# Performance work log

Hardware: AMD Instinct MI355X
Metric: run time of the kernel (lower is better)

Reference implementation:

```python
import jax, jax.numpy as jnp
import numpy as np

N_NODES = 100000
N_EDGES = 1600000
D_IN = 64
HID = 64
N_GRAPHS = 64
NEG_SLOPE = 0.2


def _glorot(k, shape):
    s = (6.0 / (shape[-2] + shape[-1])) ** 0.5
    return jax.random.uniform(k, shape, jnp.float32, -s, s)


def setup_inputs() -> dict:
    key = jax.random.key(0)
    ks = jax.random.split(key, 12)
    x = jax.random.normal(ks[0], (N_NODES, D_IN), jnp.float32)
    edge_index = jax.random.randint(ks[1], (2, N_EDGES), 0, N_NODES, dtype=jnp.int32)
    edge_attr = jax.random.normal(ks[2], (N_EDGES,), jnp.float32)
    batch = jnp.sort(jax.random.randint(ks[3], (N_NODES,), 0, N_GRAPHS, dtype=jnp.int32))
    inp = {"x": x, "edge_index": edge_index, "edge_attr": edge_attr, "batch": batch}
    dims = [(D_IN, HID), (HID, HID), (HID, HID)]
    for i, (din, dout) in enumerate(dims):
        inp[f"W{i}"] = _glorot(ks[4 + i], (din, dout))
        # att param is [1, heads=1, 2*out + nb_edge_feats=1] -> flatten to [2*out+1]
        inp[f"att{i}"] = _glorot(ks[7 + i], (1, 2 * dout + 1)).reshape(-1)
        inp[f"b{i}"] = jnp.zeros((dout,), jnp.float32)
    inp["Wf"] = _glorot(ks[10], (HID, 1))
    inp["bf"] = jnp.zeros((1,), jnp.float32)
    return inp


def _gat_layer(h, src, dst, e, valid, W, att, b, n):
    # MyGATConv (heads=1, concat=True): linear, per-edge attention logits,
    # leaky_relu, segment softmax over target nodes, weighted scatter-add.
    C = W.shape[1]
    h = h @ W                                  # [N, C]
    hi = h[dst]                                # gather target features per edge
    hj = h[src]                                # gather source features per edge
    logits = hi @ att[:C] + hj @ att[C:2 * C] + e * att[2 * C]  # [E]
    logits = jnp.where(logits >= 0, logits, NEG_SLOPE * logits)  # leaky_relu
    logits = jnp.where(valid, logits, -jnp.inf)  # drop original self-loops
    m = jax.ops.segment_max(logits, dst, num_segments=n)
    a = jnp.exp(logits - m[dst])
    a = jnp.where(valid, a, 0.0)
    denom = jax.ops.segment_sum(a, dst, num_segments=n)
    a = a / denom[dst]                         # segment softmax (self-loop guarantees denom>0)
    out = jax.ops.segment_sum(hj * a[:, None], dst, num_segments=n)
    return out + b


def reference(x, edge_index, edge_attr, batch, W0, att0, b0, W1, att1, b1, W2, att2, b2, Wf, bf):
    n = x.shape[0]
    src0, dst0 = edge_index[0], edge_index[1]
    loop = jnp.arange(n, dtype=src0.dtype)
    # remove_self_loops (via mask) + add_self_loops with edge_attr fill 0.0
    src = jnp.concatenate([src0, loop])
    dst = jnp.concatenate([dst0, loop])
    e = jnp.concatenate([edge_attr, jnp.zeros((n,), edge_attr.dtype)])
    valid = jnp.concatenate([src0 != dst0, jnp.ones((n,), bool)])
    h = x
    for (W, att, b) in ((W0, att0, b0), (W1, att1, b1), (W2, att2, b2)):
        h = jax.nn.relu(_gat_layer(h, src, dst, e, valid, W, att, b, n))
    pooled = jax.ops.segment_sum(h, batch, num_segments=N_GRAPHS)  # global_add_pool
    return (pooled @ Wf + bf).squeeze(-1)      # [N_GRAPHS]
```

## Files before the change

### kernel.cpp

```cpp
#include <hip/hip_runtime.h>
#include <math.h>

#define NNODES 100000
#define NEDGES 1600000
#define DIM 64
#define NGRAPHS 64
#define NEG_SLOPE 0.2f
#define SCAN_B 512
#define SCAN_NB ((NNODES + SCAN_B - 1) / SCAN_B)
#define MM_NB (NNODES / 16)
#define SCATTER_NB ((NEDGES / 4 + 255) / 256)


__global__ void zero_kernel(int* __restrict__ counts, float* __restrict__ pooled) {
    int i = blockIdx.x * blockDim.x + threadIdx.x;
    if (i <= NNODES) counts[i] = 0;
    if (i < NGRAPHS * DIM) pooled[i] = 0.f;
}

__global__ void hist_kernel(const int4* __restrict__ src4, const int4* __restrict__ dst4,
                            int* __restrict__ counts, int4* __restrict__ rank4) {
    int e = blockIdx.x * blockDim.x + threadIdx.x;
    if (e < NEDGES / 4) {
        int4 s = src4[e], d = dst4[e];
        int4 r;
        r.x = (s.x != d.x) ? atomicAdd(&counts[d.x], 1) : 0;
        r.y = (s.y != d.y) ? atomicAdd(&counts[d.y], 1) : 0;
        r.z = (s.z != d.z) ? atomicAdd(&counts[d.z], 1) : 0;
        r.w = (s.w != d.w) ? atomicAdd(&counts[d.w], 1) : 0;
        rank4[e] = r;
    }
}

__global__ void scan1_kernel(int* __restrict__ data, int* __restrict__ bsum) {
    __shared__ int tmp[SCAN_B];
    int t = threadIdx.x;
    int i = blockIdx.x * SCAN_B + t;
    int v = (i < NNODES) ? data[i] : 0;
    tmp[t] = v;
    __syncthreads();
    for (int off = 1; off < SCAN_B; off <<= 1) {
        int a = (t >= off) ? tmp[t - off] : 0;
        __syncthreads();
        if (t >= off) tmp[t] += a;
        __syncthreads();
    }
    if (i < NNODES) data[i] = tmp[t] - v;
    if (t == SCAN_B - 1) bsum[blockIdx.x] = tmp[t];
}

__global__ void scan2_kernel(int* __restrict__ bsum, int* __restrict__ total) {
    __shared__ int tmp[256];
    int t = threadIdx.x;
    int v = (t < SCAN_NB) ? bsum[t] : 0;
    tmp[t] = v;
    __syncthreads();
    for (int off = 1; off < 256; off <<= 1) {
        int a = (t >= off) ? tmp[t - off] : 0;
        __syncthreads();
        if (t >= off) tmp[t] += a;
        __syncthreads();
    }
    if (t < SCAN_NB) bsum[t] = tmp[t] - v;
    if (t == 255) *total = tmp[t];
}

__global__ void scan3_kernel(int* __restrict__ offs, const int* __restrict__ bsum,
                             const int* __restrict__ total) {
    int i = blockIdx.x * SCAN_B + threadIdx.x;
    if (i < NNODES) offs[i] = offs[i] + bsum[blockIdx.x];
    if (i == 0) offs[NNODES] = *total;
}

__global__ __launch_bounds__(256, 4) void scatter_mm_kernel(
        const int4* __restrict__ src4, const int4* __restrict__ dst4,
        const float4* __restrict__ eattr4, const int4* __restrict__ rank4,
        const int* __restrict__ offs, int2* __restrict__ csr,
        const float* __restrict__ hin, const float* __restrict__ W,
        const float* __restrict__ att,
        float* __restrict__ h2, float* __restrict__ ad, float* __restrict__ as_) {
    __shared__ float wl[DIM * DIM];
    __shared__ float hrow[4 * 4 * DIM];
    if (blockIdx.x < SCATTER_NB) {
        int e = blockIdx.x * 256 + threadIdx.x;
        if (e < NEDGES / 4) {
            int4 s = src4[e], d = dst4[e];
            int4 r = rank4[e];
            float4 v = eattr4[e];
            if (s.x != d.x) csr[offs[d.x] + r.x] = make_int2(s.x, __float_as_int(v.x));
            if (s.y != d.y) csr[offs[d.y] + r.y] = make_int2(s.y, __float_as_int(v.y));
            if (s.z != d.z) csr[offs[d.z] + r.z] = make_int2(s.z, __float_as_int(v.z));
            if (s.w != d.w) csr[offs[d.w] + r.w] = make_int2(s.w, __float_as_int(v.w));
        }
        return;
    }
    int blk = blockIdx.x - SCATTER_NB;
    int t = threadIdx.x;
    for (int k = t; k < DIM * DIM; k += 256) wl[k] = W[k];
    __syncthreads();
    int lane = t & 63, w = t >> 6;
    float a0 = att[lane], a1 = att[DIM + lane];
    int rbase = blk * 16 + w * 4;
    float* hw = &hrow[w * 4 * DIM];
    #pragma unroll
    for (int r = 0; r < 4; ++r)
        hw[r * DIM + lane] = hin[(size_t)(rbase + r) * DIM + lane];
    float acc0 = 0.f, acc1 = 0.f, acc2 = 0.f, acc3 = 0.f;
    #pragma unroll 16
    for (int k = 0; k < DIM; ++k) {
        float wlk = wl[k * DIM + lane];
        acc0 = fmaf(hw[0 * DIM + k], wlk, acc0);
        acc1 = fmaf(hw[1 * DIM + k], wlk, acc1);
        acc2 = fmaf(hw[2 * DIM + k], wlk, acc2);
        acc3 = fmaf(hw[3 * DIM + k], wlk, acc3);
    }
    float accs[4] = {acc0, acc1, acc2, acc3};
    #pragma unroll
    for (int r = 0; r < 4; ++r) {
        int i = rbase + r;
        float acc = accs[r];
        h2[(size_t)i * DIM + lane] = acc;
        float vd = acc * a0, vs = acc * a1;
        #pragma unroll
        for (int off = 32; off; off >>= 1) {
            vd += __shfl_xor(vd, off, 64);
            vs += __shfl_xor(vs, off, 64);
        }
        if (lane == 0) { ad[i] = vd; as_[i] = vs; }
    }
}

__global__ __launch_bounds__(256) void gat_agg_kernel(
        const float* __restrict__ h2, const float* __restrict__ ad, const float* __restrict__ as_,
        const int* __restrict__ offs, const int2* __restrict__ csr,
        const float* __restrict__ att, const float* __restrict__ bias,
        const float* __restrict__ Wnext, const float* __restrict__ attNext,
        float* __restrict__ h2next, float* __restrict__ adNext, float* __restrict__ asNext,
        float* __restrict__ hout) {
    __shared__ float wl[DIM * DIM];
    __shared__ float hrow[4 * DIM];
    int t = threadIdx.x, lane = t & 63, w = t >> 6;
    if (Wnext) {
        for (int k = t; k < DIM * DIM; k += 256) wl[k] = Wnext[k];
        __syncthreads();
    }
    float a0n = 0.f, a1n = 0.f;
    if (Wnext) { a0n = attNext[lane]; a1n = attNext[DIM + lane]; }
    int i = blockIdx.x * 4 + w;
    float att2 = att[2 * DIM];
    int beg = offs[i], end = offs[i + 1];
    float adi = ad[i];
    float ls = adi + as_[i];
    ls = ls >= 0.f ? ls : NEG_SLOPE * ls;
    float m = ls;
    float dsum = (lane == 0) ? 1.f : 0.f;
    float acc = h2[(size_t)i * DIM + lane];
    for (int e0 = beg; e0 < end; e0 += 64) {
        int e = e0 + lane;
        float l = -INFINITY;
        int s = 0;
        if (e < end) {
            int2 sv = csr[e];
            s = sv.x;
            l = adi + as_[s] + __int_as_float(sv.y) * att2;
            l = l >= 0.f ? l : NEG_SLOPE * l;
        }
        float bm = l;
        #pragma unroll
        for (int off = 32; off; off >>= 1) bm = fmaxf(bm, __shfl_xor(bm, off, 64));
        if (bm > m + 8.f) {
            float sc = __expf(m - bm);
            dsum *= sc; acc *= sc; m = bm;
        }
        float we = __expf(l - m);
        dsum += we;
        int cnt = min(64, end - e0);
        int j = 0;
        while (j + 8 <= cnt) {
            float v[8];
            #pragma unroll
            for (int k = 0; k < 8; ++k) {
                int sj = __shfl(s, j + k, 64);
                v[k] = h2[(size_t)sj * DIM + lane];
            }
            #pragma unroll
            for (int k = 0; k < 8; ++k) {
                float wgt = __shfl(we, j + k, 64);
                acc = fmaf(wgt, v[k], acc);
            }
            j += 8;
        }
        for (; j < cnt; ++j) {
            float wgt = __shfl(we, j, 64);
            int sj = __shfl(s, j, 64);
            acc = fmaf(wgt, h2[(size_t)sj * DIM + lane], acc);
        }
    }
    #pragma unroll
    for (int off = 32; off; off >>= 1) dsum += __shfl_xor(dsum, off, 64);
    float o = fmaxf(acc / dsum + bias[lane], 0.f);
    if (!Wnext) {
        hout[(size_t)i * DIM + lane] = o;
        return;
    }
    hrow[w * DIM + lane] = o;
    float h2v = 0.f;
    #pragma unroll 8
    for (int k = 0; k < DIM; ++k)
        h2v = fmaf(hrow[w * DIM + k], wl[k * DIM + lane], h2v);
    h2next[(size_t)i * DIM + lane] = h2v;
    float vd = h2v * a0n, vs = h2v * a1n;
    #pragma unroll
    for (int off = 32; off; off >>= 1) {
        vd += __shfl_xor(vd, off, 64);
        vs += __shfl_xor(vs, off, 64);
    }
    if (lane == 0) { adNext[i] = vd; asNext[i] = vs; }
}


__global__ __launch_bounds__(256) void pool_kernel(const float* __restrict__ h,
                                                   const int* __restrict__ batch,
                                                   float* __restrict__ pooled) {
    int t = threadIdx.x, lane = t & 63, w = t >> 6;
    int chunk = blockIdx.x * 4 + w;
    int i0 = chunk * 64;
    if (i0 >= NNODES) return;
    int iend = min(NNODES, i0 + 64);
    int cur = batch[i0];
    float acc = 0.f;
    for (int i = i0; i < iend; ++i) {
        int g = batch[i];
        if (g != cur) { atomicAdd(&pooled[cur * DIM + lane], acc); acc = 0.f; cur = g; }
        acc += h[(size_t)i * DIM + lane];
    }
    atomicAdd(&pooled[cur * DIM + lane], acc);
}

__global__ void final_kernel(const float* __restrict__ pooled, const float* __restrict__ Wf,
                             const float* __restrict__ bf, float* __restrict__ out) {
    int t = threadIdx.x, lane = t & 63, w = t >> 6;
    for (int g = w; g < NGRAPHS; g += 4) {
        float v = pooled[g * DIM + lane] * Wf[lane];
        #pragma unroll
        for (int off = 32; off; off >>= 1) v += __shfl_xor(v, off, 64);
        if (lane == 0) out[g] = v + bf[0];
    }
}


extern "C" void kernel_launch(void* const* d_in, const int* in_sizes, int n_in,
                              void* d_out, int out_size, void* d_ws, size_t ws_size,
                              hipStream_t stream) {
    const float* x      = (const float*)d_in[0];
    const int*   ei     = (const int*)d_in[1];
    const float* eattr  = (const float*)d_in[2];
    const int*   batch  = (const int*)d_in[3];
    const float* W[3]   = {(const float*)d_in[4], (const float*)d_in[7], (const float*)d_in[10]};
    const float* att[3] = {(const float*)d_in[5], (const float*)d_in[8], (const float*)d_in[11]};
    const float* bia[3] = {(const float*)d_in[6], (const float*)d_in[9], (const float*)d_in[12]};
    const float* Wf = (const float*)d_in[13];
    const float* bf = (const float*)d_in[14];
    float* out = (float*)d_out;
    const int* srcp = ei;
    const int* dstp = ei + NEDGES;

    char* p = (char*)d_ws;
    auto alloc = [&](size_t bytes) { char* r = p; p += (bytes + 255) & ~size_t(255); return r; };
    int*   offs    = (int*)alloc((NNODES + 1) * sizeof(int));
    int*   rank    = (int*)alloc((size_t)NEDGES * sizeof(int));
    int*   bsum    = (int*)alloc(SCAN_NB * sizeof(int));
    int*   total   = (int*)alloc(sizeof(int));
    int2*  csr     = (int2*)alloc((size_t)NEDGES * sizeof(int2));
    float* h2a     = (float*)alloc((size_t)NNODES * DIM * sizeof(float));
    float* ad_a    = (float*)alloc(NNODES * sizeof(float));
    float* as_a    = (float*)alloc(NNODES * sizeof(float));
    float* h2b     = (float*)alloc((size_t)NNODES * DIM * sizeof(float));
    float* ad_b    = (float*)alloc(NNODES * sizeof(float));
    float* as_b    = (float*)alloc(NNODES * sizeof(float));
    float* pooled  = (float*)alloc(NGRAPHS * DIM * sizeof(float));

    zero_kernel<<<(NNODES + 256) / 256, 256, 0, stream>>>(offs, pooled);
    hist_kernel<<<(NEDGES / 4 + 255) / 256, 256, 0, stream>>>(
        (const int4*)srcp, (const int4*)dstp, offs, (int4*)rank);
    scan1_kernel<<<SCAN_NB, SCAN_B, 0, stream>>>(offs, bsum);
    scan2_kernel<<<1, 256, 0, stream>>>(bsum, total);
    scan3_kernel<<<SCAN_NB, SCAN_B, 0, stream>>>(offs, bsum, total);

    scatter_mm_kernel<<<SCATTER_NB + MM_NB, 256, 0, stream>>>(
        (const int4*)srcp, (const int4*)dstp, (const float4*)eattr, (const int4*)rank,
        offs, csr, x, W[0], att[0], h2a, ad_a, as_a);

    gat_agg_kernel<<<NNODES / 4, 256, 0, stream>>>(
        h2a, ad_a, as_a, offs, csr, att[0], bia[0],
        W[1], att[1], h2b, ad_b, as_b, (float*)nullptr);
    gat_agg_kernel<<<NNODES / 4, 256, 0, stream>>>(
        h2b, ad_b, as_b, offs, csr, att[1], bia[1],
        W[2], att[2], h2a, ad_a, as_a, (float*)nullptr);
    gat_agg_kernel<<<NNODES / 4, 256, 0, stream>>>(
        h2a, ad_a, as_a, offs, csr, att[2], bia[2],
        (const float*)nullptr, (const float*)nullptr,
        (float*)nullptr, (float*)nullptr, (float*)nullptr, h2b);

    pool_kernel<<<(((NNODES + 63) / 64) + 3) / 4, 256, 0, stream>>>(h2b, batch, pooled);
    final_kernel<<<1, 256, 0, stream>>>(pooled, Wf, bf, out);
}
```

Measured before the change: 596.2 us.

## Aggregate four edges per wave with float4 gathers and LDS-staged edge weights

The GAT aggregation kernel now splits each 64-lane wave into four 16-lane groups. Each group gathers a full 256-byte source row with float4 loads, so four edges are processed per iteration, and the partial sums are combined by cross-group shuffles at the end. Edge indices and softmax weights are staged in LDS instead of being broadcast by per-edge shuffles. The max rescale now runs only when some lane crosses the threshold, and the next-layer weights are stored transposed and padded so the fused matmul can use float4 LDS reads. The trade-off is extra LDS traffic and a final reduction step per node.

```diff
diff --git a/kernel.cpp b/kernel.cpp
--- a/kernel.cpp
+++ b/kernel.cpp
@@ -10,6 +10,7 @@
 #define SCAN_NB ((NNODES + SCAN_B - 1) / SCAN_B)
 #define MM_NB (NNODES / 16)
 #define SCATTER_NB ((NEDGES / 4 + 255) / 256)
+#define WLT_S 68
 
 
 __global__ void zero_kernel(int* __restrict__ counts, float* __restrict__ pooled) {
@@ -137,24 +138,33 @@
         const float* __restrict__ Wnext, const float* __restrict__ attNext,
         float* __restrict__ h2next, float* __restrict__ adNext, float* __restrict__ asNext,
         float* __restrict__ hout) {
-    __shared__ float wl[DIM * DIM];
+    __shared__ float wlT[DIM * WLT_S];
     __shared__ float hrow[4 * DIM];
+    __shared__ int2  sw[4 * 64];
     int t = threadIdx.x, lane = t & 63, w = t >> 6;
     if (Wnext) {
-        for (int k = t; k < DIM * DIM; k += 256) wl[k] = Wnext[k];
+        for (int idx = t; idx < DIM * DIM; idx += 256) {
+            int k = idx >> 6, c = idx & 63;
+            wlT[c * WLT_S + k] = Wnext[idx];
+        }
         __syncthreads();
     }
     float a0n = 0.f, a1n = 0.f;
     if (Wnext) { a0n = attNext[lane]; a1n = attNext[DIM + lane]; }
+    int q = lane >> 4, sl = lane & 15;
+    int sl16 = sl * 16;
     int i = blockIdx.x * 4 + w;
     float att2 = att[2 * DIM];
     int beg = offs[i], end = offs[i + 1];
     float adi = ad[i];
     float ls = adi + as_[i];
-    ls = ls >= 0.f ? ls : NEG_SLOPE * ls;
+    ls = fmaxf(ls, NEG_SLOPE * ls);
     float m = ls;
     float dsum = (lane == 0) ? 1.f : 0.f;
-    float acc = h2[(size_t)i * DIM + lane];
+    float4 acc = make_float4(0.f, 0.f, 0.f, 0.f);
+    if (q == 0)
+        acc = *(const float4*)((const char*)h2 + ((size_t)i << 8) + sl16);
+    int2* swv = &sw[w * 64];
     for (int e0 = beg; e0 < end; e0 += 64) {
         int e = e0 + lane;
         float l = -INFINITY;
@@ -163,51 +173,66 @@
             int2 sv = csr[e];
             s = sv.x;
             l = adi + as_[s] + __int_as_float(sv.y) * att2;
-            l = l >= 0.f ? l : NEG_SLOPE * l;
-        }
-        float bm = l;
-        #pragma unroll
-        for (int off = 32; off; off >>= 1) bm = fmaxf(bm, __shfl_xor(bm, off, 64));
-        if (bm > m + 8.f) {
+            l = fmaxf(l, NEG_SLOPE * l);
+        }
+        if (__any(l > m + 8.f)) {
+            float bm = l;
+            #pragma unroll
+            for (int off = 32; off; off >>= 1) bm = fmaxf(bm, __shfl_xor(bm, off, 64));
             float sc = __expf(m - bm);
-            dsum *= sc; acc *= sc; m = bm;
+            dsum *= sc;
+            acc.x *= sc; acc.y *= sc; acc.z *= sc; acc.w *= sc;
+            m = bm;
         }
         float we = __expf(l - m);
         dsum += we;
-        int cnt = min(64, end - e0);
-        int j = 0;
-        while (j + 8 <= cnt) {
-            float v[8];
-            #pragma unroll
-            for (int k = 0; k < 8; ++k) {
-                int sj = __shfl(s, j + k, 64);
-                v[k] = h2[(size_t)sj * DIM + lane];
-            }
-            #pragma unroll
-            for (int k = 0; k < 8; ++k) {
-                float wgt = __shfl(we, j + k, 64);
-                acc = fmaf(wgt, v[k], acc);
-            }
-            j += 8;
-        }
-        for (; j < cnt; ++j) {
-            float wgt = __shfl(we, j, 64);
-            int sj = __shfl(s, j, 64);
-            acc = fmaf(wgt, h2[(size_t)sj * DIM + lane], acc);
-        }
+        swv[lane] = make_int2(s << 8, __float_as_int(we));
+        int cnt4 = (min(64, end - e0) + 3) >> 2;
+        for (int j = 0; j < cnt4; ++j) {
+            int2 p = swv[4 * j + q];
+            float wgt = __int_as_float(p.y);
+            float4 v = *(const float4*)((const char*)h2 + (size_t)(unsigned)p.x + sl16);
+            acc.x = fmaf(wgt, v.x, acc.x);
+            acc.y = fmaf(wgt, v.y, acc.y);
+            acc.z = fmaf(wgt, v.z, acc.z);
+            acc.w = fmaf(wgt, v.w, acc.w);
+        }
+    }
+    #pragma unroll
+    for (int off = 16; off <= 32; off <<= 1) {
+        acc.x += __shfl_xor(acc.x, off, 64);
+        acc.y += __shfl_xor(acc.y, off, 64);
+        acc.z += __shfl_xor(acc.z, off, 64);
+        acc.w += __shfl_xor(acc.w, off, 64);
     }
     #pragma unroll
     for (int off = 32; off; off >>= 1) dsum += __shfl_xor(dsum, off, 64);
-    float o = fmaxf(acc / dsum + bias[lane], 0.f);
+    float4 bi = *(const float4*)&bias[sl * 4];
+    float inv = 1.f / dsum;
+    float4 o;
+    o.x = fmaxf(fmaf(acc.x, inv, bi.x), 0.f);
+    o.y = fmaxf(fmaf(acc.y, inv, bi.y), 0.f);
+    o.z = fmaxf(fmaf(acc.z, inv, bi.z), 0.f);
+    o.w = fmaxf(fmaf(acc.w, inv, bi.w), 0.f);
     if (!Wnext) {
-        hout[(size_t)i * DIM + lane] = o;
+        if (q == 0)
+            *(float4*)((char*)hout + ((size_t)i << 8) + sl16) = o;
         return;
     }
-    hrow[w * DIM + lane] = o;
+    if (q == 0)
+        *(float4*)&hrow[w * DIM + sl * 4] = o;
     float h2v = 0.f;
-    #pragma unroll 8
-    for (int k = 0; k < DIM; ++k)
-        h2v = fmaf(hrow[w * DIM + k], wl[k * DIM + lane], h2v);
+    const float* wrow = &wlT[lane * WLT_S];
+    const float* hr = &hrow[w * DIM];
+    #pragma unroll
+    for (int k = 0; k < DIM; k += 4) {
+        float4 wv = *(const float4*)&wrow[k];
+        float4 hv = *(const float4*)&hr[k];
+        h2v = fmaf(hv.x, wv.x, h2v);
+        h2v = fmaf(hv.y, wv.y, h2v);
+        h2v = fmaf(hv.z, wv.z, h2v);
+        h2v = fmaf(hv.w, wv.w, h2v);
+    }
     h2next[(size_t)i * DIM + lane] = h2v;
     float vd = h2v * a0n, vs = h2v * a1n;
     #pragma unroll
```

Result: slower. 618.2 us (+3.7%).
